# Kernel optimization log

Hardware: AMD Instinct MI355X
Metric: run time of the kernel (lower is better)

## Reference

```python
import jax, jax.numpy as jnp
import numpy as np

N = 50000          # nodes
E = 800000         # directed edges (before self-loops)
NUM_CLASSES = 10
NEG_SLOPE = 0.2    # PyG GATConv default leaky_relu slope


def segment_softmax(logits, seg, num_segments):
    # numerically stable softmax over edges grouped by target node
    m = jax.ops.segment_max(logits, seg, num_segments=num_segments)
    e = jnp.exp(logits - m[seg])
    s = jax.ops.segment_sum(e, seg, num_segments=num_segments)
    return e / s[seg]


def gat_conv(x, src, dst, W, a_src, a_dst, b, n_nodes):
    # single-head PyG-style GATConv (eval mode: attention dropout disabled)
    h = x @ W                              # [N, C]
    alpha_src = h @ a_src                  # [N]
    alpha_dst = h @ a_dst                  # [N]
    logits = jax.nn.leaky_relu(alpha_src[src] + alpha_dst[dst], NEG_SLOPE)  # [E']
    alpha = segment_softmax(logits, dst, n_nodes)                            # [E']
    out = jax.ops.segment_sum(h[src] * alpha[:, None], dst, num_segments=n_nodes)
    return out + b


def setup_inputs() -> dict:
    key = jax.random.key(0)
    ks = jax.random.split(key, 13)
    x = jax.random.normal(ks[0], (N, 11), dtype=jnp.float32)
    edge_index = jax.random.randint(ks[1], (2, E), 0, N, dtype=jnp.int32)
    batch = jnp.zeros((N,), dtype=jnp.int32)  # unused by forward (no pooling)
    s = 0.1
    W1 = jax.random.normal(ks[2], (11, 16), jnp.float32) * s
    a1_src = jax.random.normal(ks[3], (16,), jnp.float32) * s
    a1_dst = jax.random.normal(ks[4], (16,), jnp.float32) * s
    b1 = jnp.zeros((16,), jnp.float32)
    W2 = jax.random.normal(ks[5], (16, 64), jnp.float32) * s
    a2_src = jax.random.normal(ks[6], (64,), jnp.float32) * s
    a2_dst = jax.random.normal(ks[7], (64,), jnp.float32) * s
    b2 = jnp.zeros((64,), jnp.float32)
    Wl = jax.random.normal(ks[8], (64, NUM_CLASSES), jnp.float32) * s
    bl = jnp.zeros((NUM_CLASSES,), jnp.float32)
    return {"x": x, "edge_index": edge_index, "batch": batch,
            "W1": W1, "a1_src": a1_src, "a1_dst": a1_dst, "b1": b1,
            "W2": W2, "a2_src": a2_src, "a2_dst": a2_dst, "b2": b2,
            "Wl": Wl, "bl": bl}


def reference(x, edge_index, batch, W1, a1_src, a1_dst, b1,
              W2, a2_src, a2_dst, b2, Wl, bl):
    n = x.shape[0]
    loop = jnp.arange(n, dtype=edge_index.dtype)
    src = jnp.concatenate([edge_index[0], loop])  # add self-loops (PyG default)
    dst = jnp.concatenate([edge_index[1], loop])
    h = gat_conv(x, src, dst, W1, a1_src, a1_dst, b1, n)
    h = jax.nn.relu(h)
    h = gat_conv(h, src, dst, W2, a2_src, a2_dst, b2, n)
    return h @ Wl + bl
```

## Files before the change

kernel.cpp:

```cpp
#include <hip/hip_runtime.h>
#include <hip/hip_bf16.h>
#include <hip/hip_fp16.h>

#define NEG_SLOPE 0.2f
#define BUCK 128
#define BSTRIDE 4096
#define SRCM 0x1FFFFFFu
#define SCH 2048

__device__ __forceinline__ float lrelu(float x) {
    return x > 0.f ? x : NEG_SLOPE * x;
}

__global__ __launch_bounds__(256)
void front_kernel(const float* __restrict__ x,
                  const float* __restrict__ W1,
                  const float* __restrict__ a1s, const float* __restrict__ a1d,
                  __half* __restrict__ h, float* __restrict__ as, float* __restrict__ ad,
                  int n, int tb,
                  const float* __restrict__ W2,
                  const float* __restrict__ a2s, const float* __restrict__ a2d,
                  const float* __restrict__ b2,
                  const float* __restrict__ Wl, const float* __restrict__ bl,
                  float* __restrict__ va, float* __restrict__ vd,
                  float* __restrict__ Wc, float* __restrict__ bc,
                  int* __restrict__ gcur, int nbuck) {
    const int bid = blockIdx.x;
    if (bid < tb) {
        constexpr int F_IN = 11, C_OUT = 16;
        __shared__ float sW[F_IN * C_OUT];
        __shared__ float sAs[C_OUT];
        __shared__ float sAd[C_OUT];
        for (int i = threadIdx.x; i < F_IN * C_OUT; i += 256) sW[i] = W1[i];
        if (threadIdx.x < C_OUT) { sAs[threadIdx.x] = a1s[threadIdx.x]; sAd[threadIdx.x] = a1d[threadIdx.x]; }
        __syncthreads();
        int i = bid * 256 + threadIdx.x;
        if (i >= n) return;
        float xin[F_IN];
#pragma unroll
        for (int f = 0; f < F_IN; ++f) xin[f] = x[(size_t)i * F_IN + f];
        float r[C_OUT];
        float s_acc = 0.f, d_acc = 0.f;
#pragma unroll
        for (int c = 0; c < C_OUT; ++c) {
            float acc = 0.f;
#pragma unroll
            for (int f = 0; f < F_IN; ++f) acc = fmaf(xin[f], sW[f * C_OUT + c], acc);
            r[c] = acc;
            s_acc = fmaf(acc, sAs[c], s_acc);
            d_acc = fmaf(acc, sAd[c], d_acc);
        }
        unsigned int u[8];
#pragma unroll
        for (int k = 0; k < 8; ++k) {
            __half2 hh = __floats2half2_rn(r[2 * k], r[2 * k + 1]);
            u[k] = *reinterpret_cast<unsigned int*>(&hh);
        }
        uint4* hp = reinterpret_cast<uint4*>(&h[(size_t)i * 16]);
        hp[0] = make_uint4(u[0], u[1], u[2], u[3]);
        hp[1] = make_uint4(u[4], u[5], u[6], u[7]);
        as[i] = s_acc;
        ad[i] = d_acc;
    } else {
        int t = threadIdx.x;
        for (int i = t; i < nbuck; i += 256) gcur[i] = i * BSTRIDE;
        if (t < 16) {
            float s = 0.f, s2 = 0.f;
            for (int c = 0; c < 64; ++c) {
                float w = W2[t * 64 + c];
                s = fmaf(w, a2s[c], s);
                s2 = fmaf(w, a2d[c], s2);
            }
            va[t] = s; vd[t] = s2;
        }
        int i = t - 64;
        if (i >= 0 && i < 160) {
            int f = i / 10, k = i % 10;
            float s = 0.f;
            for (int c = 0; c < 64; ++c) s = fmaf(W2[f * 64 + c], Wl[c * 10 + k], s);
            Wc[i] = s;
        }
        int k2 = t - 240;
        if (k2 >= 0 && k2 < 10) {
            float s = bl[k2];
            for (int c = 0; c < 64; ++c) s = fmaf(b2[c], Wl[c * 10 + k2], s);
            bc[k2] = s;
        }
    }
}

__global__ __launch_bounds__(256)
void scatter_kernel(const int* __restrict__ ei, int E, int ET,
                    int* __restrict__ gcur, uint2* __restrict__ pk, int nbuck,
                    const float* __restrict__ as1, const float* __restrict__ ad1) {
    __shared__ int lhist[512];
    for (int i = threadIdx.x; i < nbuck; i += 256) lhist[i] = 0;
    __syncthreads();
    const int tid = threadIdx.x;
    const int beg = blockIdx.x * SCH;

    int rs0, rs1, rs2, rs3, rs4, rs5, rs6, rs7;
    int rd0, rd1, rd2, rd3, rd4, rd5, rd6, rd7;
    const int e0 = beg + tid * 4;
    const int e1 = e0 + 1024;
    if (e0 + 3 < E) {
        const int4 s4 = *reinterpret_cast<const int4*>(&ei[e0]);
        const int4 d4 = *reinterpret_cast<const int4*>(&ei[E + e0]);
        rs0 = s4.x; rs1 = s4.y; rs2 = s4.z; rs3 = s4.w;
        rd0 = d4.x; rd1 = d4.y; rd2 = d4.z; rd3 = d4.w;
    } else {
        rs0 = rd0 = (e0 + 0 < ET) ? ((e0 + 0 < E) ? 0 : e0 + 0 - E) : -1;
        if (e0 + 0 < E) { rs0 = ei[e0 + 0]; rd0 = ei[E + e0 + 0]; }
        rs1 = rd1 = (e0 + 1 < ET) ? ((e0 + 1 < E) ? 0 : e0 + 1 - E) : -1;
        if (e0 + 1 < E) { rs1 = ei[e0 + 1]; rd1 = ei[E + e0 + 1]; }
        rs2 = rd2 = (e0 + 2 < ET) ? ((e0 + 2 < E) ? 0 : e0 + 2 - E) : -1;
        if (e0 + 2 < E) { rs2 = ei[e0 + 2]; rd2 = ei[E + e0 + 2]; }
        rs3 = rd3 = (e0 + 3 < ET) ? ((e0 + 3 < E) ? 0 : e0 + 3 - E) : -1;
        if (e0 + 3 < E) { rs3 = ei[e0 + 3]; rd3 = ei[E + e0 + 3]; }
    }
    if (e1 + 3 < E) {
        const int4 s4 = *reinterpret_cast<const int4*>(&ei[e1]);
        const int4 d4 = *reinterpret_cast<const int4*>(&ei[E + e1]);
        rs4 = s4.x; rs5 = s4.y; rs6 = s4.z; rs7 = s4.w;
        rd4 = d4.x; rd5 = d4.y; rd6 = d4.z; rd7 = d4.w;
    } else {
        rs4 = rd4 = (e1 + 0 < ET) ? ((e1 + 0 < E) ? 0 : e1 + 0 - E) : -1;
        if (e1 + 0 < E) { rs4 = ei[e1 + 0]; rd4 = ei[E + e1 + 0]; }
        rs5 = rd5 = (e1 + 1 < ET) ? ((e1 + 1 < E) ? 0 : e1 + 1 - E) : -1;
        if (e1 + 1 < E) { rs5 = ei[e1 + 1]; rd5 = ei[E + e1 + 1]; }
        rs6 = rd6 = (e1 + 2 < ET) ? ((e1 + 2 < E) ? 0 : e1 + 2 - E) : -1;
        if (e1 + 2 < E) { rs6 = ei[e1 + 2]; rd6 = ei[E + e1 + 2]; }
        rs7 = rd7 = (e1 + 3 < ET) ? ((e1 + 3 < E) ? 0 : e1 + 3 - E) : -1;
        if (e1 + 3 < E) { rs7 = ei[e1 + 3]; rd7 = ei[E + e1 + 3]; }
    }

    if (rd0 >= 0) atomicAdd(&lhist[rd0 >> 7], 1);
    if (rd1 >= 0) atomicAdd(&lhist[rd1 >> 7], 1);
    if (rd2 >= 0) atomicAdd(&lhist[rd2 >> 7], 1);
    if (rd3 >= 0) atomicAdd(&lhist[rd3 >> 7], 1);
    if (rd4 >= 0) atomicAdd(&lhist[rd4 >> 7], 1);
    if (rd5 >= 0) atomicAdd(&lhist[rd5 >> 7], 1);
    if (rd6 >= 0) atomicAdd(&lhist[rd6 >> 7], 1);
    if (rd7 >= 0) atomicAdd(&lhist[rd7 >> 7], 1);
    __syncthreads();

    for (int i = threadIdx.x; i < nbuck; i += 256) {
        int c = lhist[i];
        lhist[i] = (c > 0) ? atomicAdd(&gcur[i], c) : 0;
    }
    __syncthreads();

#define EMIT(RS, RD)                                                                   \
    if (RD >= 0) {                                                                     \
        float w = __expf(lrelu(as1[RS] + ad1[RD]));                                    \
        int slot = atomicAdd(&lhist[RD >> 7], 1);                                      \
        pk[slot] = make_uint2(((unsigned int)(RD & 127) << 25) | (unsigned int)RS,     \
                              __float_as_uint(w));                                     \
    }
    EMIT(rs0, rd0) EMIT(rs1, rd1) EMIT(rs2, rd2) EMIT(rs3, rd3)
    EMIT(rs4, rd4) EMIT(rs5, rd5) EMIT(rs6, rd6) EMIT(rs7, rd7)
#undef EMIT
}

__global__ __launch_bounds__(256)
void sortagg1_kernel(const uint2* __restrict__ pk,
                     const int* __restrict__ gcur,
                     uint2* __restrict__ cw,
                     int* __restrict__ row_beg, int* __restrict__ deg,
                     const __half* __restrict__ h,
                     const float* __restrict__ b1,
                     const float* __restrict__ va,
                     const float* __restrict__ vd,
                     __half* __restrict__ X1r,
                     float* __restrict__ as2,
                     float* __restrict__ ad2, int n) {
    __shared__ __align__(16) uint2 sbuf[BSTRIDE];
    __shared__ unsigned short sidx[BSTRIDE];
    __shared__ int lcnt[BUCK];
    __shared__ int lofs[BUCK];
    __shared__ float sb1[16], sva[16], svd[16];
    const int tid = threadIdx.x;
    const int base = blockIdx.x * BUCK;
    const int beg = blockIdx.x * BSTRIDE;
    const int cnt = gcur[blockIdx.x] - beg;

    if (tid < 16) { sb1[tid] = b1[tid]; sva[tid] = va[tid]; svd[tid] = vd[tid]; }
    if (tid < BUCK) lcnt[tid] = 0;
    for (int i = tid * 2; i < cnt; i += 512) {
        if (i + 1 < cnt) {
            *reinterpret_cast<uint4*>(&sbuf[i]) = *reinterpret_cast<const uint4*>(&pk[beg + i]);
        } else {
            sbuf[i] = pk[beg + i];
        }
    }
    __syncthreads();
    for (int i = tid; i < cnt; i += 256)
        atomicAdd(&lcnt[sbuf[i].x >> 25], 1);
    __syncthreads();
    int v = 0;
    if (tid < BUCK) { v = lcnt[tid]; lofs[tid] = v; }
    __syncthreads();
    for (int off = 1; off < BUCK; off <<= 1) {
        int u = 0;
        if (tid < BUCK && tid >= off) u = lofs[tid - off];
        __syncthreads();
        if (tid < BUCK && tid >= off) lofs[tid] += u;
        __syncthreads();
    }
    if (tid < BUCK) {
        int excl = lofs[tid] - v;
        if (base + tid < n) {
            row_beg[base + tid] = beg + excl;
            deg[base + tid] = v;
        }
        lcnt[tid] = excl;
        lofs[tid] = excl;
    }
    __syncthreads();
    for (int i = tid; i < cnt; i += 256) {
        int d = (int)(sbuf[i].x >> 25);
        int slot = atomicAdd(&lcnt[d], 1);
        sidx[slot] = (unsigned short)i;
    }
    __syncthreads();
    for (int j = tid; j < cnt; j += 256) cw[beg + j] = sbuf[sidx[j]];

    const int sg = tid >> 4;
    const int sl = tid & 15;
    const int eq = sl >> 1;
    const int cl = sl & 1;
    for (int r = 0; r < BUCK / 16; ++r) {
        int l = r * 16 + sg;
        int node = base + l;
        int nbeg = lofs[l];
        int ndeg = lcnt[l] - nbeg;
        float lsum = 0.f;
        float a0 = 0.f, a1 = 0.f, a2 = 0.f, a3 = 0.f, a4 = 0.f, a5 = 0.f, a6 = 0.f, a7 = 0.f;
        for (int chunk = 0; chunk < ndeg; chunk += 16) {
            int e = chunk + sl;
            float wv = 0.f; int sv = 0;
            if (e < ndeg) {
                uint2 rec = sbuf[sidx[nbeg + e]];
                sv = (int)(rec.x & SRCM);
                wv = __uint_as_float(rec.y);
                lsum += wv;
            }
            const int nch = min(16, ndeg - chunk);
            const int T = (nch + 7) >> 3;
            for (int t = 0; t < T; ++t) {
                int j = t * 8 + eq;
                float wj = __shfl(wv, j, 16);
                int   sj = __shfl(sv, j, 16);
                if (j < nch) {
                    uint4 hv = *reinterpret_cast<const uint4*>(&h[(size_t)sj * 16 + cl * 8]);
                    float2 f0 = __half22float2(*reinterpret_cast<__half2*>(&hv.x));
                    float2 f1 = __half22float2(*reinterpret_cast<__half2*>(&hv.y));
                    float2 f2 = __half22float2(*reinterpret_cast<__half2*>(&hv.z));
                    float2 f3 = __half22float2(*reinterpret_cast<__half2*>(&hv.w));
                    a0 = fmaf(wj, f0.x, a0); a1 = fmaf(wj, f0.y, a1);
                    a2 = fmaf(wj, f1.x, a2); a3 = fmaf(wj, f1.y, a3);
                    a4 = fmaf(wj, f2.x, a4); a5 = fmaf(wj, f2.y, a5);
                    a6 = fmaf(wj, f3.x, a6); a7 = fmaf(wj, f3.y, a7);
                }
            }
        }
#pragma unroll
        for (int k = 1; k < 16; k <<= 1) lsum += __shfl_xor(lsum, k, 16);
#pragma unroll
        for (int k = 2; k < 16; k <<= 1) {
            a0 += __shfl_xor(a0, k, 16); a1 += __shfl_xor(a1, k, 16);
            a2 += __shfl_xor(a2, k, 16); a3 += __shfl_xor(a3, k, 16);
            a4 += __shfl_xor(a4, k, 16); a5 += __shfl_xor(a5, k, 16);
            a6 += __shfl_xor(a6, k, 16); a7 += __shfl_xor(a7, k, 16);
        }
        float inv = 1.f / lsum;
        float x0 = fmaxf(fmaf(a0, inv, sb1[cl * 8 + 0]), 0.f);
        float x1 = fmaxf(fmaf(a1, inv, sb1[cl * 8 + 1]), 0.f);
        float x2 = fmaxf(fmaf(a2, inv, sb1[cl * 8 + 2]), 0.f);
        float x3 = fmaxf(fmaf(a3, inv, sb1[cl * 8 + 3]), 0.f);
        float x4 = fmaxf(fmaf(a4, inv, sb1[cl * 8 + 4]), 0.f);
        float x5 = fmaxf(fmaf(a5, inv, sb1[cl * 8 + 5]), 0.f);
        float x6 = fmaxf(fmaf(a6, inv, sb1[cl * 8 + 6]), 0.f);
        float x7 = fmaxf(fmaf(a7, inv, sb1[cl * 8 + 7]), 0.f);
        if (eq == 0 && node < n) {
            __half2 p01 = __floats2half2_rn(x0, x1);
            __half2 p23 = __floats2half2_rn(x2, x3);
            __half2 p45 = __floats2half2_rn(x4, x5);
            __half2 p67 = __floats2half2_rn(x6, x7);
            uint4 o = make_uint4(*reinterpret_cast<unsigned int*>(&p01),
                                 *reinterpret_cast<unsigned int*>(&p23),
                                 *reinterpret_cast<unsigned int*>(&p45),
                                 *reinterpret_cast<unsigned int*>(&p67));
            *reinterpret_cast<uint4*>(&X1r[(size_t)node * 16 + cl * 8]) = o;
        }
        float p = x0 * sva[cl * 8 + 0] + x1 * sva[cl * 8 + 1] + x2 * sva[cl * 8 + 2] + x3 * sva[cl * 8 + 3]
                + x4 * sva[cl * 8 + 4] + x5 * sva[cl * 8 + 5] + x6 * sva[cl * 8 + 6] + x7 * sva[cl * 8 + 7];
        float q = x0 * svd[cl * 8 + 0] + x1 * svd[cl * 8 + 1] + x2 * svd[cl * 8 + 2] + x3 * svd[cl * 8 + 3]
                + x4 * svd[cl * 8 + 4] + x5 * svd[cl * 8 + 5] + x6 * svd[cl * 8 + 6] + x7 * svd[cl * 8 + 7];
        p += __shfl_xor(p, 1, 16);
        q += __shfl_xor(q, 1, 16);
        if (sl == 0 && node < n) { as2[node] = p; ad2[node] = q; }
    }
}

__global__ void gat_agg2_kernel(const int* __restrict__ row_beg,
                                const int* __restrict__ deg,
                                const uint2* __restrict__ cw,
                                const float* __restrict__ as2,
                                const float* __restrict__ ad2,
                                const __half* __restrict__ X1r,
                                const float* __restrict__ Wc,
                                const float* __restrict__ bc,
                                float* __restrict__ out, int n) {
    __shared__ float sWc[160], sbc[10];
    for (int i = threadIdx.x; i < 160; i += blockDim.x) sWc[i] = Wc[i];
    if (threadIdx.x < 10) sbc[threadIdx.x] = bc[threadIdx.x];
    __syncthreads();
    int node = (blockIdx.x * blockDim.x + threadIdx.x) >> 4;
    int sl = threadIdx.x & 15;
    if (node >= n) return;
    int beg = row_beg[node];
    int end = beg + deg[node];
    float add = ad2[node];

    const int eq = sl >> 1;
    const int cl = sl & 1;
    float lsum = 0.f;
    float a0 = 0.f, a1 = 0.f, a2 = 0.f, a3 = 0.f, a4 = 0.f, a5 = 0.f, a6 = 0.f, a7 = 0.f;
    for (int chunk = beg; chunk < end; chunk += 16) {
        int e = chunk + sl;
        float wv = 0.f; int sv = 0;
        if (e < end) {
            sv = (int)(cw[e].x & SRCM);
            wv = __expf(lrelu(as2[sv] + add));
            lsum += wv;
        }
        const int nch = min(16, end - chunk);
        const int T = (nch + 7) >> 3;
        for (int t = 0; t < T; ++t) {
            int j = t * 8 + eq;
            float wj = __shfl(wv, j, 16);
            int   sj = __shfl(sv, j, 16);
            if (j < nch) {
                uint4 hv = *reinterpret_cast<const uint4*>(&X1r[(size_t)sj * 16 + cl * 8]);
                float2 f0 = __half22float2(*reinterpret_cast<__half2*>(&hv.x));
                float2 f1 = __half22float2(*reinterpret_cast<__half2*>(&hv.y));
                float2 f2 = __half22float2(*reinterpret_cast<__half2*>(&hv.z));
                float2 f3 = __half22float2(*reinterpret_cast<__half2*>(&hv.w));
                a0 = fmaf(wj, f0.x, a0); a1 = fmaf(wj, f0.y, a1);
                a2 = fmaf(wj, f1.x, a2); a3 = fmaf(wj, f1.y, a3);
                a4 = fmaf(wj, f2.x, a4); a5 = fmaf(wj, f2.y, a5);
                a6 = fmaf(wj, f3.x, a6); a7 = fmaf(wj, f3.y, a7);
            }
        }
    }
#pragma unroll
    for (int k = 1; k < 16; k <<= 1) lsum += __shfl_xor(lsum, k, 16);
#pragma unroll
    for (int k = 2; k < 16; k <<= 1) {
        a0 += __shfl_xor(a0, k, 16); a1 += __shfl_xor(a1, k, 16);
        a2 += __shfl_xor(a2, k, 16); a3 += __shfl_xor(a3, k, 16);
        a4 += __shfl_xor(a4, k, 16); a5 += __shfl_xor(a5, k, 16);
        a6 += __shfl_xor(a6, k, 16); a7 += __shfl_xor(a7, k, 16);
    }
    float inv = 1.f / lsum;
    a0 *= inv; a1 *= inv; a2 *= inv; a3 *= inv;
    a4 *= inv; a5 *= inv; a6 *= inv; a7 *= inv;
    float p[10];
#pragma unroll
    for (int k = 0; k < 10; ++k) {
        p[k] = a0 * sWc[(cl * 8 + 0) * 10 + k] + a1 * sWc[(cl * 8 + 1) * 10 + k]
             + a2 * sWc[(cl * 8 + 2) * 10 + k] + a3 * sWc[(cl * 8 + 3) * 10 + k]
             + a4 * sWc[(cl * 8 + 4) * 10 + k] + a5 * sWc[(cl * 8 + 5) * 10 + k]
             + a6 * sWc[(cl * 8 + 6) * 10 + k] + a7 * sWc[(cl * 8 + 7) * 10 + k];
    }
#pragma unroll
    for (int k = 0; k < 10; ++k) p[k] += __shfl_xor(p[k], 1, 16);
    if (sl < 10) {
        float v = p[0];
#pragma unroll
        for (int k = 1; k < 10; ++k) v = (sl == k) ? p[k] : v;
        out[(size_t)node * 10 + sl] = v + sbc[sl];
    }
}

extern "C" void kernel_launch(void* const* d_in, const int* in_sizes, int n_in,
                              void* d_out, int out_size, void* d_ws, size_t ws_size,
                              hipStream_t stream) {
    const float* x       = (const float*)d_in[0];
    const int*   ei      = (const int*)d_in[1];
    const float* W1      = (const float*)d_in[3];
    const float* a1_src  = (const float*)d_in[4];
    const float* a1_dst  = (const float*)d_in[5];
    const float* b1      = (const float*)d_in[6];
    const float* W2      = (const float*)d_in[7];
    const float* a2_src  = (const float*)d_in[8];
    const float* a2_dst  = (const float*)d_in[9];
    const float* b2      = (const float*)d_in[10];
    const float* Wl      = (const float*)d_in[11];
    const float* bl      = (const float*)d_in[12];
    float* out = (float*)d_out;

    const int N = in_sizes[2];
    const int E = in_sizes[1] / 2;
    const int ET = E + N;

    const int B = 256;
    auto cdiv = [](int a, int b) { return (a + b - 1) / b; };

    const int NBUCK = cdiv(N, BUCK);
    const int NBLK  = cdiv(ET, SCH);
    const int TB    = cdiv(N, B);

    char* ws = (char*)d_ws;
    size_t off = 0;
    auto alloc = [&](size_t bytes) {
        char* p = ws + off;
        off = (off + bytes + 255) & ~(size_t)255;
        return p;
    };
    __half*       h1   = (__half*)alloc((size_t)N * 16 * 2);
    __half*       X1r  = (__half*)alloc((size_t)N * 16 * 2);
    float*        as1  = (float*)alloc((size_t)N * 4);
    float*        ad1  = (float*)alloc((size_t)N * 4);
    float*        as2  = (float*)alloc((size_t)N * 4);
    float*        ad2  = (float*)alloc((size_t)N * 4);
    int*          rowb = (int*)alloc((size_t)N * 4);
    int*          degb = (int*)alloc((size_t)N * 4);
    uint2*        cw   = (uint2*)alloc((size_t)NBUCK * BSTRIDE * 8);
    uint2*        pk   = (uint2*)alloc((size_t)NBUCK * BSTRIDE * 8);
    int*          gcur = (int*)alloc((size_t)NBUCK * 4);
    float*        va   = (float*)alloc(16 * 4);
    float*        vd   = (float*)alloc(16 * 4);
    float*        Wc   = (float*)alloc(160 * 4);
    float*        bc   = (float*)alloc(10 * 4);
    (void)ws_size;

    front_kernel<<<TB + 1, B, 0, stream>>>(
        x, W1, a1_src, a1_dst, h1, as1, ad1, N, TB,
        W2, a2_src, a2_dst, b2, Wl, bl, va, vd, Wc, bc, gcur, NBUCK);

    scatter_kernel<<<NBLK, B, 0, stream>>>(ei, E, ET, gcur, pk, NBUCK, as1, ad1);

    sortagg1_kernel<<<NBUCK, 256, 0, stream>>>(pk, gcur, cw, rowb, degb,
                                               h1, b1, va, vd, X1r, as2, ad2, N);

    gat_agg2_kernel<<<cdiv(N * 16, B), B, 0, stream>>>(rowb, degb, cw, as2, ad2, X1r, Wc, bc, out, N);
}
```

Baseline: 73.66 us.

## Split fused bucket-sort/layer-1 aggregation into separate sort and aggregation kernels

```diff
diff --git a/kernel.cpp b/kernel.cpp
--- a/kernel.cpp
+++ b/kernel.cpp
@@ -163,28 +163,20 @@
 }
 
 __global__ __launch_bounds__(256)
-void sortagg1_kernel(const uint2* __restrict__ pk,
-                     const int* __restrict__ gcur,
-                     uint2* __restrict__ cw,
-                     int* __restrict__ row_beg, int* __restrict__ deg,
-                     const __half* __restrict__ h,
-                     const float* __restrict__ b1,
-                     const float* __restrict__ va,
-                     const float* __restrict__ vd,
-                     __half* __restrict__ X1r,
-                     float* __restrict__ as2,
-                     float* __restrict__ ad2, int n) {
-    __shared__ __align__(16) uint2 sbuf[BSTRIDE];
-    __shared__ unsigned short sidx[BSTRIDE];
+void bucketsort_kernel(const uint2* __restrict__ pk,
+                       const int* __restrict__ gcur,
+                       uint2* __restrict__ cw,
+                       int* __restrict__ row_beg, int* __restrict__ deg,
+                       int n) {
+    __shared__ uint2 sbuf[BSTRIDE];
+    __shared__ uint2 dbuf[BSTRIDE];
     __shared__ int lcnt[BUCK];
     __shared__ int lofs[BUCK];
-    __shared__ float sb1[16], sva[16], svd[16];
     const int tid = threadIdx.x;
     const int base = blockIdx.x * BUCK;
     const int beg = blockIdx.x * BSTRIDE;
     const int cnt = gcur[blockIdx.x] - beg;
 
-    if (tid < 16) { sb1[tid] = b1[tid]; sva[tid] = va[tid]; svd[tid] = vd[tid]; }
     if (tid < BUCK) lcnt[tid] = 0;
     for (int i = tid * 2; i < cnt; i += 512) {
         if (i + 1 < cnt) {
@@ -214,93 +206,114 @@
             deg[base + tid] = v;
         }
         lcnt[tid] = excl;
-        lofs[tid] = excl;
     }
     __syncthreads();
     for (int i = tid; i < cnt; i += 256) {
-        int d = (int)(sbuf[i].x >> 25);
-        int slot = atomicAdd(&lcnt[d], 1);
-        sidx[slot] = (unsigned short)i;
-    }
-    __syncthreads();
-    for (int j = tid; j < cnt; j += 256) cw[beg + j] = sbuf[sidx[j]];
-
-    const int sg = tid >> 4;
-    const int sl = tid & 15;
+        uint2 rec = sbuf[i];
+        int slot = atomicAdd(&lcnt[rec.x >> 25], 1);
+        dbuf[slot] = rec;
+    }
+    __syncthreads();
+    for (int i = tid * 2; i < cnt; i += 512) {
+        if (i + 1 < cnt) {
+            *reinterpret_cast<uint4*>(&cw[beg + i]) = *reinterpret_cast<uint4*>(&dbuf[i]);
+        } else {
+            cw[beg + i] = dbuf[i];
+        }
+    }
+}
+
+__global__ void gat_agg1_kernel(const int* __restrict__ row_beg,
+                                const int* __restrict__ deg,
+                                const uint2* __restrict__ cw,
+                                const __half* __restrict__ h,
+                                const float* __restrict__ b1,
+                                const float* __restrict__ va,
+                                const float* __restrict__ vd,
+                                __half* __restrict__ X1r,
+                                float* __restrict__ as2,
+                                float* __restrict__ ad2, int n) {
+    __shared__ float sb1[16], sva[16], svd[16];
+    if (threadIdx.x < 16) {
+        sb1[threadIdx.x] = b1[threadIdx.x];
+        sva[threadIdx.x] = va[threadIdx.x];
+        svd[threadIdx.x] = vd[threadIdx.x];
+    }
+    __syncthreads();
+    int node = (blockIdx.x * blockDim.x + threadIdx.x) >> 4;
+    int sl = threadIdx.x & 15;
+    if (node >= n) return;
+    int beg = row_beg[node];
+    int end = beg + deg[node];
+
     const int eq = sl >> 1;
     const int cl = sl & 1;
-    for (int r = 0; r < BUCK / 16; ++r) {
-        int l = r * 16 + sg;
-        int node = base + l;
-        int nbeg = lofs[l];
-        int ndeg = lcnt[l] - nbeg;
-        float lsum = 0.f;
-        float a0 = 0.f, a1 = 0.f, a2 = 0.f, a3 = 0.f, a4 = 0.f, a5 = 0.f, a6 = 0.f, a7 = 0.f;
-        for (int chunk = 0; chunk < ndeg; chunk += 16) {
-            int e = chunk + sl;
-            float wv = 0.f; int sv = 0;
-            if (e < ndeg) {
-                uint2 rec = sbuf[sidx[nbeg + e]];
-                sv = (int)(rec.x & SRCM);
-                wv = __uint_as_float(rec.y);
-                lsum += wv;
+    float lsum = 0.f;
+    float a0 = 0.f, a1 = 0.f, a2 = 0.f, a3 = 0.f, a4 = 0.f, a5 = 0.f, a6 = 0.f, a7 = 0.f;
+    for (int chunk = beg; chunk < end; chunk += 16) {
+        int e = chunk + sl;
+        float wv = 0.f; int sv = 0;
+        if (e < end) {
+            uint2 rec = cw[e];
+            sv = (int)(rec.x & SRCM);
+            wv = __uint_as_float(rec.y);
+            lsum += wv;
+        }
+        const int nch = min(16, end - chunk);
+        const int T = (nch + 7) >> 3;
+        for (int t = 0; t < T; ++t) {
+            int j = t * 8 + eq;
+            float wj = __shfl(wv, j, 16);
+            int   sj = __shfl(sv, j, 16);
+            if (j < nch) {
+                uint4 hv = *reinterpret_cast<const uint4*>(&h[(size_t)sj * 16 + cl * 8]);
+                float2 f0 = __half22float2(*reinterpret_cast<__half2*>(&hv.x));
+                float2 f1 = __half22float2(*reinterpret_cast<__half2*>(&hv.y));
+                float2 f2 = __half22float2(*reinterpret_cast<__half2*>(&hv.z));
+                float2 f3 = __half22float2(*reinterpret_cast<__half2*>(&hv.w));
+                a0 = fmaf(wj, f0.x, a0); a1 = fmaf(wj, f0.y, a1);
+                a2 = fmaf(wj, f1.x, a2); a3 = fmaf(wj, f1.y, a3);
+                a4 = fmaf(wj, f2.x, a4); a5 = fmaf(wj, f2.y, a5);
+                a6 = fmaf(wj, f3.x, a6); a7 = fmaf(wj, f3.y, a7);
             }
-            const int nch = min(16, ndeg - chunk);
-            const int T = (nch + 7) >> 3;
-            for (int t = 0; t < T; ++t) {
-                int j = t * 8 + eq;
-                float wj = __shfl(wv, j, 16);
-                int   sj = __shfl(sv, j, 16);
-                if (j < nch) {
-                    uint4 hv = *reinterpret_cast<const uint4*>(&h[(size_t)sj * 16 + cl * 8]);
-                    float2 f0 = __half22float2(*reinterpret_cast<__half2*>(&hv.x));
-                    float2 f1 = __half22float2(*reinterpret_cast<__half2*>(&hv.y));
-                    float2 f2 = __half22float2(*reinterpret_cast<__half2*>(&hv.z));
-                    float2 f3 = __half22float2(*reinterpret_cast<__half2*>(&hv.w));
-                    a0 = fmaf(wj, f0.x, a0); a1 = fmaf(wj, f0.y, a1);
-                    a2 = fmaf(wj, f1.x, a2); a3 = fmaf(wj, f1.y, a3);
-                    a4 = fmaf(wj, f2.x, a4); a5 = fmaf(wj, f2.y, a5);
-                    a6 = fmaf(wj, f3.x, a6); a7 = fmaf(wj, f3.y, a7);
-                }
-            }
-        }
-#pragma unroll
-        for (int k = 1; k < 16; k <<= 1) lsum += __shfl_xor(lsum, k, 16);
-#pragma unroll
-        for (int k = 2; k < 16; k <<= 1) {
-            a0 += __shfl_xor(a0, k, 16); a1 += __shfl_xor(a1, k, 16);
-            a2 += __shfl_xor(a2, k, 16); a3 += __shfl_xor(a3, k, 16);
-            a4 += __shfl_xor(a4, k, 16); a5 += __shfl_xor(a5, k, 16);
-            a6 += __shfl_xor(a6, k, 16); a7 += __shfl_xor(a7, k, 16);
-        }
-        float inv = 1.f / lsum;
-        float x0 = fmaxf(fmaf(a0, inv, sb1[cl * 8 + 0]), 0.f);
-        float x1 = fmaxf(fmaf(a1, inv, sb1[cl * 8 + 1]), 0.f);
-        float x2 = fmaxf(fmaf(a2, inv, sb1[cl * 8 + 2]), 0.f);
-        float x3 = fmaxf(fmaf(a3, inv, sb1[cl * 8 + 3]), 0.f);
-        float x4 = fmaxf(fmaf(a4, inv, sb1[cl * 8 + 4]), 0.f);
-        float x5 = fmaxf(fmaf(a5, inv, sb1[cl * 8 + 5]), 0.f);
-        float x6 = fmaxf(fmaf(a6, inv, sb1[cl * 8 + 6]), 0.f);
-        float x7 = fmaxf(fmaf(a7, inv, sb1[cl * 8 + 7]), 0.f);
-        if (eq == 0 && node < n) {
-            __half2 p01 = __floats2half2_rn(x0, x1);
-            __half2 p23 = __floats2half2_rn(x2, x3);
-            __half2 p45 = __floats2half2_rn(x4, x5);
-            __half2 p67 = __floats2half2_rn(x6, x7);
-            uint4 o = make_uint4(*reinterpret_cast<unsigned int*>(&p01),
-                                 *reinterpret_cast<unsigned int*>(&p23),
-                                 *reinterpret_cast<unsigned int*>(&p45),
-                                 *reinterpret_cast<unsigned int*>(&p67));
-            *reinterpret_cast<uint4*>(&X1r[(size_t)node * 16 + cl * 8]) = o;
-        }
-        float p = x0 * sva[cl * 8 + 0] + x1 * sva[cl * 8 + 1] + x2 * sva[cl * 8 + 2] + x3 * sva[cl * 8 + 3]
-                + x4 * sva[cl * 8 + 4] + x5 * sva[cl * 8 + 5] + x6 * sva[cl * 8 + 6] + x7 * sva[cl * 8 + 7];
-        float q = x0 * svd[cl * 8 + 0] + x1 * svd[cl * 8 + 1] + x2 * svd[cl * 8 + 2] + x3 * svd[cl * 8 + 3]
-                + x4 * svd[cl * 8 + 4] + x5 * svd[cl * 8 + 5] + x6 * svd[cl * 8 + 6] + x7 * svd[cl * 8 + 7];
-        p += __shfl_xor(p, 1, 16);
-        q += __shfl_xor(q, 1, 16);
-        if (sl == 0 && node < n) { as2[node] = p; ad2[node] = q; }
-    }
+        }
+    }
+#pragma unroll
+    for (int k = 1; k < 16; k <<= 1) lsum += __shfl_xor(lsum, k, 16);
+#pragma unroll
+    for (int k = 2; k < 16; k <<= 1) {
+        a0 += __shfl_xor(a0, k, 16); a1 += __shfl_xor(a1, k, 16);
+        a2 += __shfl_xor(a2, k, 16); a3 += __shfl_xor(a3, k, 16);
+        a4 += __shfl_xor(a4, k, 16); a5 += __shfl_xor(a5, k, 16);
+        a6 += __shfl_xor(a6, k, 16); a7 += __shfl_xor(a7, k, 16);
+    }
+    float inv = 1.f / lsum;
+    float x0 = fmaxf(fmaf(a0, inv, sb1[cl * 8 + 0]), 0.f);
+    float x1 = fmaxf(fmaf(a1, inv, sb1[cl * 8 + 1]), 0.f);
+    float x2 = fmaxf(fmaf(a2, inv, sb1[cl * 8 + 2]), 0.f);
+    float x3 = fmaxf(fmaf(a3, inv, sb1[cl * 8 + 3]), 0.f);
+    float x4 = fmaxf(fmaf(a4, inv, sb1[cl * 8 + 4]), 0.f);
+    float x5 = fmaxf(fmaf(a5, inv, sb1[cl * 8 + 5]), 0.f);
+    float x6 = fmaxf(fmaf(a6, inv, sb1[cl * 8 + 6]), 0.f);
+    float x7 = fmaxf(fmaf(a7, inv, sb1[cl * 8 + 7]), 0.f);
+    if (eq == 0) {
+        __half2 p01 = __floats2half2_rn(x0, x1);
+        __half2 p23 = __floats2half2_rn(x2, x3);
+        __half2 p45 = __floats2half2_rn(x4, x5);
+        __half2 p67 = __floats2half2_rn(x6, x7);
+        uint4 o = make_uint4(*reinterpret_cast<unsigned int*>(&p01),
+                             *reinterpret_cast<unsigned int*>(&p23),
+                             *reinterpret_cast<unsigned int*>(&p45),
+                             *reinterpret_cast<unsigned int*>(&p67));
+        *reinterpret_cast<uint4*>(&X1r[(size_t)node * 16 + cl * 8]) = o;
+    }
+    float p = x0 * sva[cl * 8 + 0] + x1 * sva[cl * 8 + 1] + x2 * sva[cl * 8 + 2] + x3 * sva[cl * 8 + 3]
+            + x4 * sva[cl * 8 + 4] + x5 * sva[cl * 8 + 5] + x6 * sva[cl * 8 + 6] + x7 * sva[cl * 8 + 7];
+    float q = x0 * svd[cl * 8 + 0] + x1 * svd[cl * 8 + 1] + x2 * svd[cl * 8 + 2] + x3 * svd[cl * 8 + 3]
+            + x4 * svd[cl * 8 + 4] + x5 * svd[cl * 8 + 5] + x6 * svd[cl * 8 + 6] + x7 * svd[cl * 8 + 7];
+    p += __shfl_xor(p, 1, 16);
+    q += __shfl_xor(q, 1, 16);
+    if (sl == 0) { as2[node] = p; ad2[node] = q; }
 }
 
 __global__ void gat_agg2_kernel(const int* __restrict__ row_beg,
@@ -442,8 +455,9 @@
 
     scatter_kernel<<<NBLK, B, 0, stream>>>(ei, E, ET, gcur, pk, NBUCK, as1, ad1);
 
-    sortagg1_kernel<<<NBUCK, 256, 0, stream>>>(pk, gcur, cw, rowb, degb,
-                                               h1, b1, va, vd, X1r, as2, ad2, N);
+    bucketsort_kernel<<<NBUCK, 256, 0, stream>>>(pk, gcur, cw, rowb, degb, N);
+
+    gat_agg1_kernel<<<cdiv(N * 16, B), B, 0, stream>>>(rowb, degb, cw, h1, b1, va, vd, X1r, as2, ad2, N);
 
     gat_agg2_kernel<<<cdiv(N * 16, B), B, 0, stream>>>(rowb, degb, cw, as2, ad2, X1r, Wc, bc, out, N);
 }
```

Measured after the change: 71.52 us. -2.9%, faster.
